# Kernel tuning notes

Measured on AMD Instinct MI355X. Metric: run time of the kernel, lower is better.

The kernel has to match this reference:

```python
import jax, jax.numpy as jnp
import numpy as np

TOP_K = 4

def _silu_and_mul(gu):
    g, u = jnp.split(gu, 2, axis=-1)
    return jax.nn.silu(g) * u

def setup_inputs() -> dict:
    key = jax.random.key(0)
    ks = jax.random.split(key, 7)
    H, E, I, Is = 2048, 16, 1408, 5632
    s = 0.02
    return {
        "hidden_states": jax.random.normal(ks[0], (4, 1024, H), dtype=jnp.float32),
        "gate_w": jax.random.normal(ks[1], (E, H), dtype=jnp.float32) * s,
        "sgate_w": jax.random.normal(ks[2], (1, H), dtype=jnp.float32) * s,
        "w13": jax.random.normal(ks[3], (E, 2 * I, H), dtype=jnp.float32) * s,
        "w2": jax.random.normal(ks[4], (E, H, I), dtype=jnp.float32) * s,
        "shared_gate_up_w": jax.random.normal(ks[5], (2 * Is, H), dtype=jnp.float32) * s,
        "shared_down_w": jax.random.normal(ks[6], (H, Is), dtype=jnp.float32) * s,
    }

def reference(hidden_states, gate_w, sgate_w, w13, w2, shared_gate_up_w, shared_down_w):
    B, S, H = hidden_states.shape
    x = hidden_states.reshape(-1, H)  # [M, H]
    E = gate_w.shape[0]

    # shared expert: SiluAndMul MLP gated by sigmoid(shared_expert_gate(x))
    shared = _silu_and_mul(x @ shared_gate_up_w.T) @ shared_down_w.T
    shared = shared * jax.nn.sigmoid(x @ sgate_w.T)  # [M, H]

    # router: softmax in fp32, top-k (NOT renormalized, per original code)
    router_logits = x @ gate_w.T
    routing_weights = jax.nn.softmax(router_logits.astype(jnp.float32), axis=-1)
    topk_w, topk_ids = jax.lax.top_k(routing_weights, TOP_K)  # [M, K]

    # loop over fixed expert set via scan; every token goes through each
    # expert, masked by its routing coefficient (0 if not routed)
    def body(acc, ew):
        w13_e, w2_e, e = ew
        coef = jnp.sum(jnp.where(topk_ids == e, topk_w, 0.0), axis=-1)  # [M]
        h = _silu_and_mul(x @ w13_e.T)  # [M, I]
        acc = acc + (h @ w2_e.T).astype(jnp.float32) * coef[:, None]
        return acc, None

    init = jnp.zeros((x.shape[0], H), dtype=jnp.float32)
    sparse_out, _ = jax.lax.scan(body, init, (w13, w2, jnp.arange(E)))
    out = shared + sparse_out.astype(x.dtype)
    return out.reshape(B, S, H)
```

## Files before the change

### kernel.cpp

```cpp
#include <hip/hip_runtime.h>
#include <hip/hip_bf16.h>

#define E_NUM 16
#define TOPK 4
#define H_DIM 2048
#define I_DIM 1408
#define IS_DIM 5632
#define M_TOK 4096

typedef __attribute__((ext_vector_type(8))) short short8;
typedef __attribute__((ext_vector_type(4))) float f32x4;

static __device__ __forceinline__ unsigned short f2bf(float f) {
    unsigned int u = __float_as_uint(f);
    unsigned int r = (u + 0x7FFFu + ((u >> 16) & 1u)) >> 16;
    return (unsigned short)r;
}

static __device__ __forceinline__ void gl16(const unsigned short* g, unsigned short* l) {
    __builtin_amdgcn_global_load_lds(
        (const __attribute__((address_space(1))) unsigned int*)g,
        (__attribute__((address_space(3))) unsigned int*)l, 16, 0, 0);
}

__global__ __launch_bounds__(256) void k_router(
    const float* __restrict__ x, const float* __restrict__ gw,
    const float* __restrict__ sgw, int* __restrict__ counts,
    int* __restrict__ ltok, float* __restrict__ lcoef, float* __restrict__ sg)
{
    const int wid = threadIdx.x >> 6, lane = threadIdx.x & 63;
    const int t = blockIdx.x * 4 + wid;
    const float* xr = x + (size_t)t * H_DIM;
    float xv[32];
#pragma unroll
    for (int i = 0; i < 32; ++i) xv[i] = xr[i * 64 + lane];

    float lg[E_NUM];
    for (int e = 0; e < E_NUM; ++e) {
        const float* g = gw + (size_t)e * H_DIM;
        float s = 0.f;
#pragma unroll
        for (int i = 0; i < 32; ++i) s += xv[i] * g[i * 64 + lane];
#pragma unroll
        for (int off = 32; off; off >>= 1) s += __shfl_xor(s, off);
        lg[e] = s;
    }
    {
        float s = 0.f;
#pragma unroll
        for (int i = 0; i < 32; ++i) s += xv[i] * sgw[i * 64 + lane];
#pragma unroll
        for (int off = 32; off; off >>= 1) s += __shfl_xor(s, off);
        if (lane == 0) sg[t] = 1.f / (1.f + __expf(-s));
    }
    float mx = lg[0];
#pragma unroll
    for (int e = 1; e < E_NUM; ++e) mx = fmaxf(mx, lg[e]);
    float sum = 0.f, w[E_NUM];
#pragma unroll
    for (int e = 0; e < E_NUM; ++e) { w[e] = __expf(lg[e] - mx); sum += w[e]; }
    float inv = 1.f / sum;
#pragma unroll
    for (int e = 0; e < E_NUM; ++e) w[e] *= inv;

    if (lane == 0) {
        for (int j = 0; j < TOPK; ++j) {
            float best = -1.f; int bi = 0;
            for (int e = 0; e < E_NUM; ++e) if (w[e] > best) { best = w[e]; bi = e; }
            int pos = atomicAdd(&counts[bi], 1);
            ltok[bi * M_TOK + pos]  = t;
            lcoef[bi * M_TOK + pos] = best;
            w[bi] = -2.f;
        }
    }
}

__global__ void k_prefix(const int* __restrict__ counts, int* __restrict__ base) {
    if (threadIdx.x == 0) {
        int a = 0;
        for (int e = 0; e < E_NUM; ++e) { base[e] = a; a += counts[e]; }
        base[E_NUM] = a;
    }
}

__global__ __launch_bounds__(256) void k_cvtw(const float* __restrict__ src,
                                              unsigned short* __restrict__ dst, size_t n8)
{
    size_t stride = (size_t)gridDim.x * 256;
    for (size_t t = (size_t)blockIdx.x * 256 + threadIdx.x; t < n8; t += stride) {
        size_t i = t * 8;
        float4 a = *(const float4*)(src + i);
        float4 b = *(const float4*)(src + i + 4);
        union { unsigned short u[8]; short8 v; } o;
        o.u[0] = f2bf(a.x); o.u[1] = f2bf(a.y); o.u[2] = f2bf(a.z); o.u[3] = f2bf(a.w);
        o.u[4] = f2bf(b.x); o.u[5] = f2bf(b.y); o.u[6] = f2bf(b.z); o.u[7] = f2bf(b.w);
        *(short8*)(dst + i) = o.v;
    }
}

template<int MODE, int BN, int KDIM, int NOFF, long long BSTR, bool BCVT>
__global__ __launch_bounds__(256) void k_gemm(
    const unsigned short* __restrict__ Abase,
    const void* __restrict__ Bvoid,
    void* __restrict__ outp,
    const int* __restrict__ ltok, const float* __restrict__ lcoef,
    const int* __restrict__ counts, const int* __restrict__ basearr,
    const float* __restrict__ sg)
{
    constexpr bool DUAL = (MODE == 0 || MODE == 2);
    constexpr int NFR = BN / 32;

    const int tid = threadIdx.x;
    const int lane = tid & 63, wid = tid >> 6;
    const int wr = wid >> 1, wc = wid & 1;
    const int lr = lane & 15, lk = lane >> 4;
    const int n0 = blockIdx.x * BN;
    const int r0 = blockIdx.y * 128;
    const int e = blockIdx.z;

    int cnt = M_TOK, gbase = 0;
    if constexpr (MODE == 2 || MODE == 3) {
        cnt = counts[e];
        if (r0 >= cnt) return;
        gbase = basearr[e];
    }

    __shared__ unsigned short sA[128 * 64];
    __shared__ unsigned short sB[128 * 64];

    const int srow = lane >> 3, sc8 = lane & 7;
    const unsigned short* aptr[4];
#pragma unroll
    for (int i = 0; i < 4; ++i) {
        const int row = (i * 4 + wid) * 8 + srow;
        int ar;
        if constexpr (MODE == 0 || MODE == 1) ar = r0 + row;
        else if constexpr (MODE == 2) {
            int rr = r0 + row; if (rr > cnt - 1) rr = cnt - 1;
            ar = ltok[e * M_TOK + rr];
        } else {
            int rr = r0 + row; if (rr > cnt - 1) rr = cnt - 1;
            ar = gbase + rr;
        }
        aptr[i] = Abase + (size_t)ar * KDIM + ((sc8 ^ (row & 7)) << 3);
    }
    const unsigned short* bptr[4];
    const float* Bf = nullptr;
    if constexpr (BCVT) {
        const unsigned short* Bx = (const unsigned short*)Bvoid + (size_t)e * (size_t)BSTR;
#pragma unroll
        for (int i = 0; i < 4; ++i) {
            const int row = (i * 4 + wid) * 8 + srow;
            int br;
            if constexpr (DUAL) br = (row >= 64) ? (NOFF + n0 + row - 64) : (n0 + row);
            else br = n0 + row;
            bptr[i] = Bx + (size_t)br * KDIM + ((sc8 ^ (row & 7)) << 3);
        }
    } else {
        Bf = (const float*)Bvoid + (size_t)e * (size_t)BSTR;
    }

    f32x4 acc[4][NFR];
    f32x4 accu[4][NFR];
    const f32x4 z = {0.f, 0.f, 0.f, 0.f};
#pragma unroll
    for (int m = 0; m < 4; ++m)
#pragma unroll
        for (int n = 0; n < NFR; ++n) { acc[m][n] = z; if constexpr (DUAL) accu[m][n] = z; }

#pragma unroll 1
    for (int kt = 0; kt < KDIM; kt += 64) {
#pragma unroll
        for (int i = 0; i < 4; ++i)
            gl16(aptr[i] + kt, &sA[(i * 4 + wid) * 512]);
        if constexpr (BCVT) {
#pragma unroll
            for (int i = 0; i < 4; ++i)
                gl16(bptr[i] + kt, &sB[(i * 4 + wid) * 512]);
        } else {
#pragma unroll
            for (int i = 0; i < 4; ++i) {
                int c = i * 256 + tid;
                int row = c >> 3, c8 = c & 7;
                int br;
                if constexpr (DUAL) br = (row >= 64) ? (NOFF + n0 + row - 64) : (n0 + row);
                else br = n0 + row;
                const float* bs = Bf + (size_t)br * KDIM + kt + c8 * 8;
                float4 f0 = *(const float4*)bs;
                float4 f1 = *(const float4*)(bs + 4);
                union { unsigned short u[8]; short8 v; } o;
                o.u[0] = f2bf(f0.x); o.u[1] = f2bf(f0.y); o.u[2] = f2bf(f0.z); o.u[3] = f2bf(f0.w);
                o.u[4] = f2bf(f1.x); o.u[5] = f2bf(f1.y); o.u[6] = f2bf(f1.z); o.u[7] = f2bf(f1.w);
                *(short8*)&sB[(row << 6) + ((c8 ^ (row & 7)) << 3)] = o.v;
            }
        }
        __syncthreads();
#pragma unroll
        for (int kk = 0; kk < 2; ++kk) {
            const int c8 = kk * 4 + lk;
            short8 af[4];
#pragma unroll
            for (int m = 0; m < 4; ++m) {
                int row = wr * 64 + m * 16 + lr;
                af[m] = *(const short8*)&sA[(row << 6) + ((c8 ^ (row & 7)) << 3)];
            }
#pragma unroll
            for (int n = 0; n < NFR; ++n) {
                int rowb = wc * (BN / 2) + n * 16 + lr;
                short8 bf = *(const short8*)&sB[(rowb << 6) + ((c8 ^ (rowb & 7)) << 3)];
#pragma unroll
                for (int m = 0; m < 4; ++m)
                    acc[m][n] = __builtin_amdgcn_mfma_f32_16x16x32_bf16(af[m], bf, acc[m][n], 0, 0, 0);
                if constexpr (DUAL) {
                    int rowu = rowb + 64;
                    short8 bu = *(const short8*)&sB[(rowu << 6) + ((c8 ^ (rowu & 7)) << 3)];
#pragma unroll
                    for (int m = 0; m < 4; ++m)
                        accu[m][n] = __builtin_amdgcn_mfma_f32_16x16x32_bf16(af[m], bu, accu[m][n], 0, 0, 0);
                }
            }
        }
        __syncthreads();
    }

    const int colbase = n0 + wc * (BN / 2);
#pragma unroll
    for (int m = 0; m < 4; ++m) {
#pragma unroll
        for (int j = 0; j < 4; ++j) {
            const int r = wr * 64 + m * 16 + lk * 4 + j;
            if constexpr (MODE == 0) {
                size_t orow = (size_t)(r0 + r) * IS_DIM;
#pragma unroll
                for (int n = 0; n < NFR; ++n) {
                    int col = colbase + n * 16 + lr;
                    float g = acc[m][n][j];
                    float h = g / (1.f + __expf(-g)) * accu[m][n][j];
                    ((unsigned short*)outp)[orow + col] = f2bf(h);
                }
            } else if constexpr (MODE == 2) {
                if (r0 + r < cnt) {
                    size_t orow = (size_t)(gbase + r0 + r) * I_DIM;
#pragma unroll
                    for (int n = 0; n < NFR; ++n) {
                        int col = colbase + n * 16 + lr;
                        float g = acc[m][n][j];
                        float h = g / (1.f + __expf(-g)) * accu[m][n][j];
                        ((unsigned short*)outp)[orow + col] = f2bf(h);
                    }
                }
            } else if constexpr (MODE == 1) {
                int tok = r0 + r;
                float scale = sg[tok];
                size_t orow = (size_t)tok * H_DIM;
#pragma unroll
                for (int n = 0; n < NFR; ++n) {
                    int col = colbase + n * 16 + lr;
                    ((float*)outp)[orow + col] = acc[m][n][j] * scale;
                }
            } else {
                if (r0 + r < cnt) {
                    int tok = ltok[e * M_TOK + r0 + r];
                    float scale = lcoef[e * M_TOK + r0 + r];
                    size_t orow = (size_t)tok * H_DIM;
#pragma unroll
                    for (int n = 0; n < NFR; ++n) {
                        int col = colbase + n * 16 + lr;
                        atomicAdd((float*)outp + orow + col, acc[m][n][j] * scale);
                    }
                }
            }
        }
    }
}

extern "C" void kernel_launch(void* const* d_in, const int* in_sizes, int n_in,
                              void* d_out, int out_size, void* d_ws, size_t ws_size,
                              hipStream_t stream) {
    const float* x    = (const float*)d_in[0];
    const float* gw   = (const float*)d_in[1];
    const float* sgw  = (const float*)d_in[2];
    const float* w13  = (const float*)d_in[3];
    const float* w2   = (const float*)d_in[4];
    const float* sguw = (const float*)d_in[5];
    const float* sdw  = (const float*)d_in[6];
    float* out = (float*)d_out;

    char* ws = (char*)d_ws;
    unsigned short* xb   = (unsigned short*)ws;
    unsigned short* hbuf = (unsigned short*)(ws + 16777216);
    const bool full = (ws_size >= 409485824ULL);
    unsigned short* w13b  = (unsigned short*)(ws + 62914560);
    unsigned short* w2b   = (unsigned short*)(ws + 247463936);
    unsigned short* sguwb = (unsigned short*)(ws + 339738624);
    unsigned short* sdwb  = (unsigned short*)(ws + 385875968);
    size_t so = full ? 408944640ULL : 62914560ULL;
    int*   ltok   = (int*)  (ws + so);
    float* lcoef  = (float*)(ws + so + 262144);
    int*   counts = (int*)  (ws + so + 524288);
    int*   basep  = (int*)  (ws + so + 524288 + 256);
    float* sg     = (float*)(ws + so + 524288 + 512);

    hipMemsetAsync(counts, 0, 64, stream);
    k_router<<<M_TOK / 4, 256, 0, stream>>>(x, gw, sgw, counts, ltok, lcoef, sg);
    k_prefix<<<1, 64, 0, stream>>>(counts, basep);
    k_cvtw<<<4096, 256, 0, stream>>>(x, xb, (size_t)M_TOK * H_DIM / 8);

    if (full) {
        k_cvtw<<<8192, 256, 0, stream>>>(sguw, sguwb, (size_t)2 * IS_DIM * H_DIM / 8);
        k_cvtw<<<8192, 256, 0, stream>>>(sdw,  sdwb,  (size_t)H_DIM * IS_DIM / 8);
        k_cvtw<<<8192, 256, 0, stream>>>(w13,  w13b,  (size_t)E_NUM * 2 * I_DIM * H_DIM / 8);
        k_cvtw<<<8192, 256, 0, stream>>>(w2,   w2b,   (size_t)E_NUM * H_DIM * I_DIM / 8);

        k_gemm<0, 64, 2048, IS_DIM, 0, true>
            <<<dim3(IS_DIM / 64, M_TOK / 128, 1), 256, 0, stream>>>(
                xb, sguwb, hbuf, ltok, lcoef, counts, basep, sg);
        k_gemm<1, 128, 5632, 0, 0, true>
            <<<dim3(H_DIM / 128, M_TOK / 128, 1), 256, 0, stream>>>(
                hbuf, sdwb, out, ltok, lcoef, counts, basep, sg);
        k_gemm<2, 64, 2048, I_DIM, 5767168LL, true>
            <<<dim3(I_DIM / 64, M_TOK / 128, E_NUM), 256, 0, stream>>>(
                xb, w13b, hbuf, ltok, lcoef, counts, basep, sg);
        k_gemm<3, 128, 1408, 0, 2883584LL, true>
            <<<dim3(H_DIM / 128, M_TOK / 128, E_NUM), 256, 0, stream>>>(
                hbuf, w2b, out, ltok, lcoef, counts, basep, sg);
    } else {
        k_gemm<0, 64, 2048, IS_DIM, 0, false>
            <<<dim3(IS_DIM / 64, M_TOK / 128, 1), 256, 0, stream>>>(
                xb, sguw, hbuf, ltok, lcoef, counts, basep, sg);
        k_gemm<1, 128, 5632, 0, 0, false>
            <<<dim3(H_DIM / 128, M_TOK / 128, 1), 256, 0, stream>>>(
                hbuf, sdw, out, ltok, lcoef, counts, basep, sg);
        k_gemm<2, 64, 2048, I_DIM, 5767168LL, false>
            <<<dim3(I_DIM / 64, M_TOK / 128, E_NUM), 256, 0, stream>>>(
                xb, w13, hbuf, ltok, lcoef, counts, basep, sg);
        k_gemm<3, 128, 1408, 0, 2883584LL, false>
            <<<dim3(H_DIM / 128, M_TOK / 128, E_NUM), 256, 0, stream>>>(
                hbuf, w2, out, ltok, lcoef, counts, basep, sg);
    }
}
```

Before: 1.337 ms.

## Enlarge GEMM tiles to 256 rows with double-buffered LDS, XCD remap and split-K

Reworks the MoE and shared-expert GEMMs to use 512-thread blocks with 256-row tiles, 8x NFR accumulators per wave, and double-buffered dynamic LDS prefetching the next K-slice while computing the current one. Workgroups are remapped across XCDs for L2 locality. The shared down projection is split along K over two z-slices and accumulated with atomics into a pre-zeroed output. The fp32-weight fallback path is removed, so the full workspace is now always assumed. The aim is more MFMA reuse per LDS load and hidden global latency, at the cost of higher register/LDS pressure and extra atomic traffic plus an output memset.

```diff
diff --git a/kernel.cpp b/kernel.cpp
--- a/kernel.cpp
+++ b/kernel.cpp
@@ -98,25 +98,37 @@
     }
 }
 
-template<int MODE, int BN, int KDIM, int NOFF, long long BSTR, bool BCVT>
-__global__ __launch_bounds__(256) void k_gemm(
+template<int MODE, int BN, int KDIM, int NOFF, long long BSTR, int KSPLIT>
+__global__ __launch_bounds__(512, 2) void k_gemm(
     const unsigned short* __restrict__ Abase,
-    const void* __restrict__ Bvoid,
+    const unsigned short* __restrict__ Bbase,
     void* __restrict__ outp,
     const int* __restrict__ ltok, const float* __restrict__ lcoef,
     const int* __restrict__ counts, const int* __restrict__ basearr,
     const float* __restrict__ sg)
 {
     constexpr bool DUAL = (MODE == 0 || MODE == 2);
-    constexpr int NFR = BN / 32;
+    constexpr int NFR = BN / 64;
+    constexpr int KCH = KDIM / KSPLIT;
+
+    extern __shared__ unsigned short smem[];
+    unsigned short* sA = smem;
+    unsigned short* sB = smem + 32768;
 
     const int tid = threadIdx.x;
     const int lane = tid & 63, wid = tid >> 6;
-    const int wr = wid >> 1, wc = wid & 1;
+    const int wr = wid >> 2, wcol = wid & 3;
     const int lr = lane & 15, lk = lane >> 4;
-    const int n0 = blockIdx.x * BN;
-    const int r0 = blockIdx.y * 128;
-    const int e = blockIdx.z;
+
+    const unsigned gx = gridDim.x, gy = gridDim.y;
+    const unsigned nwg = gx * gy;
+    const unsigned orig = blockIdx.y * gx + blockIdx.x;
+    const unsigned q8 = nwg >> 3, r8 = nwg & 7;
+    const unsigned xcd = orig & 7, off8 = orig >> 3;
+    const unsigned wg = ((xcd < r8) ? xcd * (q8 + 1) : r8 * (q8 + 1) + (xcd - r8) * q8) + off8;
+    const int n0 = (int)(wg / gy) * BN;
+    const int r0 = (int)(wg % gy) * 256;
+    const int e  = blockIdx.z;
 
     int cnt = M_TOK, gbase = 0;
     if constexpr (MODE == 2 || MODE == 3) {
@@ -124,111 +136,87 @@
         if (r0 >= cnt) return;
         gbase = basearr[e];
     }
-
-    __shared__ unsigned short sA[128 * 64];
-    __shared__ unsigned short sB[128 * 64];
-
-    const int srow = lane >> 3, sc8 = lane & 7;
+    const int kbeg = (KSPLIT > 1) ? e * KCH : 0;
+    const unsigned short* Bexp = Bbase + (size_t)e * (size_t)BSTR;
+
     const unsigned short* aptr[4];
+    const unsigned short* bptr[4];
 #pragma unroll
     for (int i = 0; i < 4; ++i) {
-        const int row = (i * 4 + wid) * 8 + srow;
+        const int c = i * 512 + tid;
+        const int row = c >> 3, c8 = c & 7;
         int ar;
         if constexpr (MODE == 0 || MODE == 1) ar = r0 + row;
-        else if constexpr (MODE == 2) {
+        else {
             int rr = r0 + row; if (rr > cnt - 1) rr = cnt - 1;
-            ar = ltok[e * M_TOK + rr];
-        } else {
-            int rr = r0 + row; if (rr > cnt - 1) rr = cnt - 1;
-            ar = gbase + rr;
+            ar = (MODE == 2) ? ltok[e * M_TOK + rr] : (gbase + rr);
         }
-        aptr[i] = Abase + (size_t)ar * KDIM + ((sc8 ^ (row & 7)) << 3);
-    }
-    const unsigned short* bptr[4];
-    const float* Bf = nullptr;
-    if constexpr (BCVT) {
-        const unsigned short* Bx = (const unsigned short*)Bvoid + (size_t)e * (size_t)BSTR;
-#pragma unroll
-        for (int i = 0; i < 4; ++i) {
-            const int row = (i * 4 + wid) * 8 + srow;
-            int br;
-            if constexpr (DUAL) br = (row >= 64) ? (NOFF + n0 + row - 64) : (n0 + row);
-            else br = n0 + row;
-            bptr[i] = Bx + (size_t)br * KDIM + ((sc8 ^ (row & 7)) << 3);
-        }
-    } else {
-        Bf = (const float*)Bvoid + (size_t)e * (size_t)BSTR;
-    }
-
-    f32x4 acc[4][NFR];
-    f32x4 accu[4][NFR];
+        aptr[i] = Abase + (size_t)ar * KDIM + kbeg + ((c8 ^ (row & 7)) << 3);
+        int br;
+        if constexpr (DUAL) br = (row < 128) ? (n0 + row) : (NOFF + n0 + row - 128);
+        else br = n0 + row;
+        bptr[i] = Bexp + (size_t)br * KDIM + kbeg + ((c8 ^ (row & 7)) << 3);
+    }
+
+    f32x4 acc[8][NFR];
+    f32x4 accu[DUAL ? 8 : 1][NFR];
     const f32x4 z = {0.f, 0.f, 0.f, 0.f};
 #pragma unroll
-    for (int m = 0; m < 4; ++m)
+    for (int m = 0; m < 8; ++m)
 #pragma unroll
         for (int n = 0; n < NFR; ++n) { acc[m][n] = z; if constexpr (DUAL) accu[m][n] = z; }
 
+    auto STAGE = [&](int buf, int kt) {
+        const int bo = buf << 14;
+#pragma unroll
+        for (int i = 0; i < 4; ++i) gl16(aptr[i] + kt, &sA[bo + ((i * 512 + tid) << 3)]);
+#pragma unroll
+        for (int i = 0; i < 4; ++i) gl16(bptr[i] + kt, &sB[bo + ((i * 512 + tid) << 3)]);
+    };
+
+    STAGE(0, 0);
+    __syncthreads();
+    int cur = 0;
 #pragma unroll 1
-    for (int kt = 0; kt < KDIM; kt += 64) {
-#pragma unroll
-        for (int i = 0; i < 4; ++i)
-            gl16(aptr[i] + kt, &sA[(i * 4 + wid) * 512]);
-        if constexpr (BCVT) {
-#pragma unroll
-            for (int i = 0; i < 4; ++i)
-                gl16(bptr[i] + kt, &sB[(i * 4 + wid) * 512]);
-        } else {
-#pragma unroll
-            for (int i = 0; i < 4; ++i) {
-                int c = i * 256 + tid;
-                int row = c >> 3, c8 = c & 7;
-                int br;
-                if constexpr (DUAL) br = (row >= 64) ? (NOFF + n0 + row - 64) : (n0 + row);
-                else br = n0 + row;
-                const float* bs = Bf + (size_t)br * KDIM + kt + c8 * 8;
-                float4 f0 = *(const float4*)bs;
-                float4 f1 = *(const float4*)(bs + 4);
-                union { unsigned short u[8]; short8 v; } o;
-                o.u[0] = f2bf(f0.x); o.u[1] = f2bf(f0.y); o.u[2] = f2bf(f0.z); o.u[3] = f2bf(f0.w);
-                o.u[4] = f2bf(f1.x); o.u[5] = f2bf(f1.y); o.u[6] = f2bf(f1.z); o.u[7] = f2bf(f1.w);
-                *(short8*)&sB[(row << 6) + ((c8 ^ (row & 7)) << 3)] = o.v;
+    for (int kt = 0; kt < KCH; kt += 64) {
+        if (kt + 64 < KCH) STAGE(cur ^ 1, kt + 64);
+        __builtin_amdgcn_s_setprio(1);
+#pragma unroll
+        for (int kk = 0; kk < 2; ++kk) {
+            const int c8 = kk * 4 + lk;
+            short8 af[8];
+#pragma unroll
+            for (int m = 0; m < 8; ++m) {
+                const int row = wr * 128 + m * 16 + lr;
+                af[m] = *(const short8*)&sA[(cur << 14) + (row << 6) + ((c8 ^ (row & 7)) << 3)];
+            }
+#pragma unroll
+            for (int n = 0; n < NFR; ++n) {
+                const int rowb = wcol * (BN / 4) + n * 16 + lr;
+                short8 bf = *(const short8*)&sB[(cur << 14) + (rowb << 6) + ((c8 ^ (rowb & 7)) << 3)];
+#pragma unroll
+                for (int m = 0; m < 8; ++m)
+                    acc[m][n] = __builtin_amdgcn_mfma_f32_16x16x32_bf16(af[m], bf, acc[m][n], 0, 0, 0);
+                if constexpr (DUAL) {
+                    const int rowu = rowb + 128;
+                    short8 bu = *(const short8*)&sB[(cur << 14) + (rowu << 6) + ((c8 ^ (rowu & 7)) << 3)];
+#pragma unroll
+                    for (int m = 0; m < 8; ++m)
+                        accu[m][n] = __builtin_amdgcn_mfma_f32_16x16x32_bf16(af[m], bu, accu[m][n], 0, 0, 0);
+                }
             }
         }
+        __builtin_amdgcn_s_setprio(0);
         __syncthreads();
-#pragma unroll
-        for (int kk = 0; kk < 2; ++kk) {
-            const int c8 = kk * 4 + lk;
-            short8 af[4];
-#pragma unroll
-            for (int m = 0; m < 4; ++m) {
-                int row = wr * 64 + m * 16 + lr;
-                af[m] = *(const short8*)&sA[(row << 6) + ((c8 ^ (row & 7)) << 3)];
-            }
-#pragma unroll
-            for (int n = 0; n < NFR; ++n) {
-                int rowb = wc * (BN / 2) + n * 16 + lr;
-                short8 bf = *(const short8*)&sB[(rowb << 6) + ((c8 ^ (rowb & 7)) << 3)];
-#pragma unroll
-                for (int m = 0; m < 4; ++m)
-                    acc[m][n] = __builtin_amdgcn_mfma_f32_16x16x32_bf16(af[m], bf, acc[m][n], 0, 0, 0);
-                if constexpr (DUAL) {
-                    int rowu = rowb + 64;
-                    short8 bu = *(const short8*)&sB[(rowu << 6) + ((c8 ^ (rowu & 7)) << 3)];
-#pragma unroll
-                    for (int m = 0; m < 4; ++m)
-                        accu[m][n] = __builtin_amdgcn_mfma_f32_16x16x32_bf16(af[m], bu, accu[m][n], 0, 0, 0);
-                }
-            }
-        }
-        __syncthreads();
-    }
-
-    const int colbase = n0 + wc * (BN / 2);
-#pragma unroll
-    for (int m = 0; m < 4; ++m) {
+        cur ^= 1;
+    }
+
+    const int colbase = n0 + wcol * (BN / 4);
+#pragma unroll
+    for (int m = 0; m < 8; ++m) {
 #pragma unroll
         for (int j = 0; j < 4; ++j) {
-            const int r = wr * 64 + m * 16 + lk * 4 + j;
+            const int r = wr * 128 + m * 16 + lk * 4 + j;
             if constexpr (MODE == 0) {
                 size_t orow = (size_t)(r0 + r) * IS_DIM;
 #pragma unroll
@@ -256,7 +244,7 @@
 #pragma unroll
                 for (int n = 0; n < NFR; ++n) {
                     int col = colbase + n * 16 + lr;
-                    ((float*)outp)[orow + col] = acc[m][n][j] * scale;
+                    atomicAdd((float*)outp + orow + col, acc[m][n][j] * scale);
                 }
             } else {
                 if (r0 + r < cnt) {
@@ -287,14 +275,13 @@
     float* out = (float*)d_out;
 
     char* ws = (char*)d_ws;
-    unsigned short* xb   = (unsigned short*)ws;
-    unsigned short* hbuf = (unsigned short*)(ws + 16777216);
-    const bool full = (ws_size >= 409485824ULL);
+    unsigned short* xb    = (unsigned short*)ws;
+    unsigned short* hbuf  = (unsigned short*)(ws + 16777216);
     unsigned short* w13b  = (unsigned short*)(ws + 62914560);
     unsigned short* w2b   = (unsigned short*)(ws + 247463936);
     unsigned short* sguwb = (unsigned short*)(ws + 339738624);
     unsigned short* sdwb  = (unsigned short*)(ws + 385875968);
-    size_t so = full ? 408944640ULL : 62914560ULL;
+    size_t so = 408944640ULL;
     int*   ltok   = (int*)  (ws + so);
     float* lcoef  = (float*)(ws + so + 262144);
     int*   counts = (int*)  (ws + so + 524288);
@@ -302,40 +289,35 @@
     float* sg     = (float*)(ws + so + 524288 + 512);
 
     hipMemsetAsync(counts, 0, 64, stream);
+    hipMemsetAsync(out, 0, (size_t)out_size * sizeof(float), stream);
     k_router<<<M_TOK / 4, 256, 0, stream>>>(x, gw, sgw, counts, ltok, lcoef, sg);
     k_prefix<<<1, 64, 0, stream>>>(counts, basep);
     k_cvtw<<<4096, 256, 0, stream>>>(x, xb, (size_t)M_TOK * H_DIM / 8);
-
-    if (full) {
-        k_cvtw<<<8192, 256, 0, stream>>>(sguw, sguwb, (size_t)2 * IS_DIM * H_DIM / 8);
-        k_cvtw<<<8192, 256, 0, stream>>>(sdw,  sdwb,  (size_t)H_DIM * IS_DIM / 8);
-        k_cvtw<<<8192, 256, 0, stream>>>(w13,  w13b,  (size_t)E_NUM * 2 * I_DIM * H_DIM / 8);
-        k_cvtw<<<8192, 256, 0, stream>>>(w2,   w2b,   (size_t)E_NUM * H_DIM * I_DIM / 8);
-
-        k_gemm<0, 64, 2048, IS_DIM, 0, true>
-            <<<dim3(IS_DIM / 64, M_TOK / 128, 1), 256, 0, stream>>>(
-                xb, sguwb, hbuf, ltok, lcoef, counts, basep, sg);
-        k_gemm<1, 128, 5632, 0, 0, true>
-            <<<dim3(H_DIM / 128, M_TOK / 128, 1), 256, 0, stream>>>(
-                hbuf, sdwb, out, ltok, lcoef, counts, basep, sg);
-        k_gemm<2, 64, 2048, I_DIM, 5767168LL, true>
-            <<<dim3(I_DIM / 64, M_TOK / 128, E_NUM), 256, 0, stream>>>(
-                xb, w13b, hbuf, ltok, lcoef, counts, basep, sg);
-        k_gemm<3, 128, 1408, 0, 2883584LL, true>
-            <<<dim3(H_DIM / 128, M_TOK / 128, E_NUM), 256, 0, stream>>>(
-                hbuf, w2b, out, ltok, lcoef, counts, basep, sg);
-    } else {
-        k_gemm<0, 64, 2048, IS_DIM, 0, false>
-            <<<dim3(IS_DIM / 64, M_TOK / 128, 1), 256, 0, stream>>>(
-                xb, sguw, hbuf, ltok, lcoef, counts, basep, sg);
-        k_gemm<1, 128, 5632, 0, 0, false>
-            <<<dim3(H_DIM / 128, M_TOK / 128, 1), 256, 0, stream>>>(
-                hbuf, sdw, out, ltok, lcoef, counts, basep, sg);
-        k_gemm<2, 64, 2048, I_DIM, 5767168LL, false>
-            <<<dim3(I_DIM / 64, M_TOK / 128, E_NUM), 256, 0, stream>>>(
-                xb, w13, hbuf, ltok, lcoef, counts, basep, sg);
-        k_gemm<3, 128, 1408, 0, 2883584LL, false>
-            <<<dim3(H_DIM / 128, M_TOK / 128, E_NUM), 256, 0, stream>>>(
-                hbuf, w2, out, ltok, lcoef, counts, basep, sg);
-    }
-}
+    k_cvtw<<<8192, 256, 0, stream>>>(sguw, sguwb, (size_t)2 * IS_DIM * H_DIM / 8);
+    k_cvtw<<<8192, 256, 0, stream>>>(sdw,  sdwb,  (size_t)H_DIM * IS_DIM / 8);
+    k_cvtw<<<8192, 256, 0, stream>>>(w13,  w13b,  (size_t)E_NUM * 2 * I_DIM * H_DIM / 8);
+    k_cvtw<<<8192, 256, 0, stream>>>(w2,   w2b,   (size_t)E_NUM * H_DIM * I_DIM / 8);
+
+    static const int DYN = 131072;
+    (void)hipFuncSetAttribute(reinterpret_cast<const void*>(&k_gemm<0, 128, 2048, IS_DIM, 0LL, 1>),
+                              hipFuncAttributeMaxDynamicSharedMemorySize, DYN);
+    (void)hipFuncSetAttribute(reinterpret_cast<const void*>(&k_gemm<1, 256, 5632, 0, 0LL, 2>),
+                              hipFuncAttributeMaxDynamicSharedMemorySize, DYN);
+    (void)hipFuncSetAttribute(reinterpret_cast<const void*>(&k_gemm<2, 128, 2048, I_DIM, 5767168LL, 1>),
+                              hipFuncAttributeMaxDynamicSharedMemorySize, DYN);
+    (void)hipFuncSetAttribute(reinterpret_cast<const void*>(&k_gemm<3, 256, 1408, 0, 2883584LL, 1>),
+                              hipFuncAttributeMaxDynamicSharedMemorySize, DYN);
+
+    k_gemm<0, 128, 2048, IS_DIM, 0LL, 1>
+        <<<dim3(IS_DIM / 128, M_TOK / 256, 1), 512, DYN, stream>>>(
+            xb, sguwb, hbuf, ltok, lcoef, counts, basep, sg);
+    k_gemm<1, 256, 5632, 0, 0LL, 2>
+        <<<dim3(H_DIM / 256, M_TOK / 256, 2), 512, DYN, stream>>>(
+            hbuf, sdwb, out, ltok, lcoef, counts, basep, sg);
+    k_gemm<2, 128, 2048, I_DIM, 5767168LL, 1>
+        <<<dim3(I_DIM / 128, M_TOK / 256, E_NUM), 512, DYN, stream>>>(
+            xb, w13b, hbuf, ltok, lcoef, counts, basep, sg);
+    k_gemm<3, 256, 1408, 0, 2883584LL, 1>
+        <<<dim3(H_DIM / 256, M_TOK / 256, E_NUM), 512, DYN, stream>>>(
+            hbuf, w2b, out, ltok, lcoef, counts, basep, sg);
+}
```

New measurement: 1.215 ms. -9.1%, faster.
